# Optimization experiments

Measured on AMD Instinct MI355X. Metric: run time of the kernel, lower is better.

The kernel has to match this reference:

```python
import jax, jax.numpy as jnp
import numpy as np

D_MODEL = 1024
N_HEADS = 16
D_K = D_MODEL // N_HEADS
SEQ = 2048
BATCH = 4
THETA = 10000.0


def setup_inputs() -> dict:
    key = jax.random.key(0)
    k_x, k_q, k_k, k_v, k_o = jax.random.split(key, 5)
    std = (2.0 / (D_MODEL + D_MODEL)) ** 0.5
    def trunc(k):
        # truncated normal on [-3*std, 3*std]
        return std * jax.random.truncated_normal(k, -3.0, 3.0, (D_MODEL, D_MODEL), jnp.float32)
    return {
        "x": jax.random.normal(k_x, (BATCH, SEQ, D_MODEL), jnp.float32),
        "token_positions": jnp.arange(SEQ, dtype=jnp.int32),
        "Wq": trunc(k_q),
        "Wk": trunc(k_k),
        "Wv": trunc(k_v),
        "Wo": trunc(k_o),
    }


def _rope(x, cos, sin):
    # x: [b, h, s, d_k]; cos/sin: [s, d_k/2] broadcast over b,h
    x_even = x[..., ::2]
    x_odd = x[..., 1::2]
    out_even = x_even * cos - x_odd * sin
    out_odd = x_even * sin + x_odd * cos
    # interleave back: stack -> [..., d_k/2, 2] -> [..., d_k]
    return jnp.stack([out_even, out_odd], axis=-1).reshape(x.shape)


def reference(x, token_positions, Wq, Wk, Wv, Wo):
    B, S, D = x.shape
    H, dk = N_HEADS, D_K

    def proj(W):
        y = jnp.einsum("bsi,oi->bso", x, W)
        return y.reshape(B, S, H, dk).transpose(0, 2, 1, 3)  # b h s d

    q, k, v = proj(Wq), proj(Wk), proj(Wv)

    # RoPE caches
    freq = 1.0 / THETA ** (jnp.arange(0, dk, 2, dtype=jnp.float32) / dk)  # [dk/2]
    pos = token_positions.astype(jnp.float32)  # [S]
    freqs = pos[:, None] * freq[None, :]  # [S, dk/2]
    cos, sin = jnp.cos(freqs), jnp.sin(freqs)
    q = _rope(q, cos, sin)
    k = _rope(k, cos, sin)

    scale = 1.0 / jnp.sqrt(jnp.float32(dk))
    scores = jnp.einsum("bhqd,bhkd->bhqk", q, k) * scale  # [b,h,S,S]
    causal = jnp.tril(jnp.ones((S, S), dtype=bool))
    scores = jnp.where(causal, scores, -jnp.inf)
    # naive stable softmax (max-subtract / exp / sum), matching source
    s_max = jnp.max(scores, axis=-1, keepdims=True)
    e = jnp.exp(scores - s_max)
    attn = e / jnp.sum(e, axis=-1, keepdims=True)
    out = jnp.einsum("bhqk,bhkd->bhqd", attn, v)  # [b,h,S,dk]
    out = out.transpose(0, 2, 1, 3).reshape(B, S, D)
    return jnp.einsum("bsi,oi->bso", out, Wo)
```

## Files before the change

### kernel.cpp

```cpp
#include <hip/hip_runtime.h>

#define SEQ   2048
#define BATCH 4
#define NH    16
#define DM    1024
#define MTOT  (BATCH*SEQ)

typedef unsigned short u16;
typedef unsigned int   u32;
typedef __attribute__((ext_vector_type(8)))  __bf16 bf16x8;
typedef __attribute__((ext_vector_type(4)))  float  f32x4;
typedef __attribute__((ext_vector_type(16))) float  f32x16;
typedef __attribute__((address_space(1))) u32 as1_u32;
typedef __attribute__((address_space(3))) u32 as3_u32;

__device__ __forceinline__ u16 f2bf(float f) {
  union { float f; u32 u; } c; c.f = f;
  return (u16)((c.u + 0x7fffu + ((c.u >> 16) & 1u)) >> 16);
}

__global__ __launch_bounds__(256)
void prep_k(const float* __restrict__ x,  const float* __restrict__ Wq,
            const float* __restrict__ Wk, const float* __restrict__ Wv,
            const float* __restrict__ Wo, const int* __restrict__ pos,
            u16* __restrict__ xb,  u16* __restrict__ wqb, u16* __restrict__ wkb,
            u16* __restrict__ wvb, u16* __restrict__ wob, float2* __restrict__ tab) {
  const int NX4 = MTOT * DM / 4;
  const int NW4 = DM * DM / 4;
  const int i = blockIdx.x * blockDim.x + threadIdx.x;
  int j = i;
  const float* src = nullptr; u16* dst = nullptr;
  if (j < NX4) { src = x; dst = xb; }
  else {
    j -= NX4;
    if (j < NW4) { src = Wq; dst = wqb; }
    else if (j < 2 * NW4) { src = Wk; dst = wkb; j -= NW4; }
    else if (j < 3 * NW4) { src = Wv; dst = wvb; j -= 2 * NW4; }
    else if (j < 4 * NW4) { src = Wo; dst = wob; j -= 3 * NW4; }
    else {
      j -= 4 * NW4;
      if (j < SEQ * 32) {
        const int s = j >> 5, jj = j & 31;
        const float p = (float)pos[s];
        const float fr = powf(10000.f, -(float)jj / 32.f);
        tab[j] = make_float2(cosf(p * fr), sinf(p * fr));
      }
      return;
    }
  }
  float4 v = reinterpret_cast<const float4*>(src)[j];
  ushort4 o;
  o.x = f2bf(v.x); o.y = f2bf(v.y); o.z = f2bf(v.z); o.w = f2bf(v.w);
  reinterpret_cast<ushort4*>(dst)[j] = o;
}

template<int EPI>
__global__ __launch_bounds__(256)
void gemm_bt(const u16* __restrict__ A,
             const u16* __restrict__ B0, const u16* __restrict__ B1, const u16* __restrict__ B2,
             float* __restrict__ outF,
             u16* __restrict__ Qh, u16* __restrict__ Kh, u16* __restrict__ Vt,
             const float2* __restrict__ tab) {
  const int K = DM, N = DM;
  __shared__ u16 lsA[128 * 32];
  __shared__ u16 lsB[128 * 32];
  const int t = threadIdx.x;
  const int lane = t & 63;
  const int wid = t >> 6;
  const int wr = wid >> 1, wc = wid & 1;
  const int m0 = blockIdx.y * 128, n0 = blockIdx.x * 128;
  const int z = blockIdx.z;
  const u16* Bt = (z == 0) ? B0 : (z == 1 ? B1 : B2);

  f32x4 acc[4][4] = {};

  const int srow = t >> 2;
  const int scol = (t & 3) * 8;
  const u16* gA = A + (size_t)(m0 + srow) * K + scol;
  const u16* gB = Bt + (size_t)(n0 + srow) * K + scol;
  const u32 lo = (u32)t * 16u;

  for (int kt = 0; kt < K; kt += 32) {
    __builtin_amdgcn_global_load_lds((const as1_u32*)(gA + kt),
                                     (as3_u32*)((char*)lsA + lo), 16, 0, 0);
    __builtin_amdgcn_global_load_lds((const as1_u32*)(gA + (size_t)64 * K + kt),
                                     (as3_u32*)((char*)lsA + 4096 + lo), 16, 0, 0);
    __builtin_amdgcn_global_load_lds((const as1_u32*)(gB + kt),
                                     (as3_u32*)((char*)lsB + lo), 16, 0, 0);
    __builtin_amdgcn_global_load_lds((const as1_u32*)(gB + (size_t)64 * K + kt),
                                     (as3_u32*)((char*)lsB + 4096 + lo), 16, 0, 0);
    __syncthreads();
    bf16x8 af[4], bfr[4];
#pragma unroll
    for (int mt = 0; mt < 4; ++mt)
      af[mt] = *(const bf16x8*)&lsA[(wr * 64 + mt * 16 + (lane & 15)) * 32 + (lane >> 4) * 8];
#pragma unroll
    for (int nt = 0; nt < 4; ++nt)
      bfr[nt] = *(const bf16x8*)&lsB[(wc * 64 + nt * 16 + (lane & 15)) * 32 + (lane >> 4) * 8];
#pragma unroll
    for (int mt = 0; mt < 4; ++mt)
#pragma unroll
      for (int nt = 0; nt < 4; ++nt)
        acc[mt][nt] = __builtin_amdgcn_mfma_f32_16x16x32_bf16(af[mt], bfr[nt], acc[mt][nt], 0, 0, 0);
    __syncthreads();
  }

#pragma unroll
  for (int mt = 0; mt < 4; ++mt) {
    const int gmb = m0 + wr * 64 + mt * 16 + (lane >> 4) * 4;
#pragma unroll
    for (int nt = 0; nt < 4; ++nt) {
      const int gn = n0 + wc * 64 + nt * 16 + (lane & 15);
#pragma unroll
      for (int r = 0; r < 4; ++r) {
        float v = acc[mt][nt][r];
        if (EPI == 0) {
          outF[(size_t)(gmb + r) * N + gn] = v;
        } else {
          const int row = gmb + r;
          const int b = row >> 11, s = row & (SEQ - 1);
          const int h = gn >> 6, dd = gn & 63;
          if (z < 2) {
            float p = __shfl_xor(v, 1);
            const float2 cs = tab[(s << 5) + (dd >> 1)];
            float o = ((lane & 1) == 0) ? (v * cs.x - p * cs.y) : (p * cs.y + v * cs.x);
            if (z == 0) o *= 0.18033688011112042f;
            u16* dst = z ? Kh : Qh;
            dst[((size_t)((b * NH + h) * SEQ + s) << 6) + dd] = f2bf(o);
          } else {
            Vt[((size_t)((b * NH + h) << 6) + dd) * SEQ + s] = f2bf(v);
          }
        }
      }
    }
  }
}

__global__ __launch_bounds__(256)
void attn_k(const u16* __restrict__ Qh, const u16* __restrict__ Kh,
            const u16* __restrict__ Vt, u16* __restrict__ AO) {
  __shared__ u16 lsK[2][64 * 64];
  __shared__ u16 lsV[2][64 * 64];
  const int t = threadIdx.x, lane = t & 63, w = t >> 6;
  const int hiL = lane >> 5;
  const int q31 = lane & 31;
  const int bid = blockIdx.x;
  const int bh = bid & 63, b = bh >> 4, h = bh & 15;
  const int chunk_blk = 15 - (bid >> 6);
  const int qb_blk = chunk_blk * 128;
  const int tendB = (qb_blk + 127) >> 6;
  const int qbase = qb_blk + w * 32;
  const int tendW = (qbase + 31) >> 6;
  const u16* Qp = Qh + (size_t)bh * SEQ * 64;
  const u16* Kp = Kh + (size_t)bh * SEQ * 64;
  const u16* Vp = Vt + (size_t)bh * 64 * SEQ;

  bf16x8 qa[4];
#pragma unroll
  for (int kc = 0; kc < 4; ++kc)
    qa[kc] = *(const bf16x8*)(Qp + (size_t)(qbase + q31) * 64 + kc * 16 + hiL * 8);

  f32x16 O0 = {}, O1 = {};
  float m = -1e30f, l = 0.f;

#define STAGE(bf, kt_)                                                                  \
  {                                                                                     \
    const int k0s = (kt_) * 64;                                                         \
    _Pragma("unroll")                                                                   \
    for (int hh = 0; hh < 2; ++hh) {                                                    \
      const int idx = hh * 256 + t;                                                     \
      const int row = idx >> 3;                                                         \
      const int cb = ((idx & 7) << 4) ^ ((row & 7) << 4);                               \
      __builtin_amdgcn_global_load_lds((const as1_u32*)(Kp + (size_t)(k0s + row) * 64 + (cb >> 1)), \
                                       (as3_u32*)((char*)&lsK[bf][0] + idx * 16), 16, 0, 0); \
      __builtin_amdgcn_global_load_lds((const as1_u32*)(Vp + (size_t)row * SEQ + k0s + (cb >> 1)), \
                                       (as3_u32*)((char*)&lsV[bf][0] + idx * 16), 16, 0, 0); \
    }                                                                                   \
  }

  STAGE(0, 0)
  STAGE(1, 1)

  for (int kt = 0; kt <= tendB; ++kt) {
    const int cur = kt & 1;
    asm volatile("s_waitcnt vmcnt(4)" ::: "memory");
    __builtin_amdgcn_sched_barrier(0);
    __builtin_amdgcn_s_barrier();

    if (kt <= tendW) {
      const int k0 = kt * 64;
      const int swz = (q31 & 7) << 4;

      f32x16 S0 = {}, S1 = {};
#pragma unroll
      for (int kc = 0; kc < 4; ++kc) {
        const int cb = (kc * 32 + hiL * 16) ^ swz;
        bf16x8 ka = *(const bf16x8*)&lsK[cur][q31 * 64 + (cb >> 1)];
        S0 = __builtin_amdgcn_mfma_f32_32x32x16_bf16(ka, qa[kc], S0, 0, 0, 0);
      }
#pragma unroll
      for (int kc = 0; kc < 4; ++kc) {
        const int cb = (kc * 32 + hiL * 16) ^ swz;
        bf16x8 ka = *(const bf16x8*)&lsK[cur][(32 + q31) * 64 + (cb >> 1)];
        S1 = __builtin_amdgcn_mfma_f32_32x32x16_bf16(ka, qa[kc], S1, 0, 0, 0);
      }

      if (kt == tendW) {
        const int qg = qbase + q31;
#pragma unroll
        for (int r = 0; r < 16; ++r) {
          const int kg = k0 + (r & 3) + 8 * (r >> 2) + 4 * hiL;
          S0[r] = (kg > qg) ? -1e30f : S0[r];
          S1[r] = (kg + 32 > qg) ? -1e30f : S1[r];
        }
      }

      float vmax = -1e30f;
#pragma unroll
      for (int r = 0; r < 16; ++r) {
        vmax = fmaxf(vmax, S0[r]);
        vmax = fmaxf(vmax, S1[r]);
      }
      vmax = fmaxf(vmax, __shfl_xor(vmax, 32));

      if (vmax > m + 7.f) {
        const float al = exp2f(m - vmax);
        m = vmax; l *= al;
#pragma unroll
        for (int r = 0; r < 16; ++r) { O0[r] *= al; O1[r] *= al; }
      }

      float rs = 0.f;
#pragma unroll
      for (int r = 0; r < 16; ++r) {
        const float p0 = exp2f(S0[r] - m);
        const float p1 = exp2f(S1[r] - m);
        S0[r] = p0; S1[r] = p1;
        rs += p0 + p1;
      }
      l += rs;

      bf16x8 pb[4];
#define PACKKC(SV, kb, OUT)                                                         \
      {                                                                             \
        u32 qL0, qL1, qH0, qH1;                                                     \
        asm("v_cvt_pk_bf16_f32 %0, %1, %2" : "=v"(qL0) : "v"(SV[8*(kb)+0]), "v"(SV[8*(kb)+1])); \
        asm("v_cvt_pk_bf16_f32 %0, %1, %2" : "=v"(qL1) : "v"(SV[8*(kb)+2]), "v"(SV[8*(kb)+3])); \
        asm("v_cvt_pk_bf16_f32 %0, %1, %2" : "=v"(qH0) : "v"(SV[8*(kb)+4]), "v"(SV[8*(kb)+5])); \
        asm("v_cvt_pk_bf16_f32 %0, %1, %2" : "=v"(qH1) : "v"(SV[8*(kb)+6]), "v"(SV[8*(kb)+7])); \
        const u32 sA = hiL ? qL0 : qH0;                                             \
        const u32 sB = hiL ? qL1 : qH1;                                             \
        const u32 rA = (u32)__shfl_xor((int)sA, 32);                                \
        const u32 rB = (u32)__shfl_xor((int)sB, 32);                                \
        union { u32 wds[4]; bf16x8 v; } uu;                                         \
        uu.wds[0] = hiL ? rA : qL0;                                                 \
        uu.wds[1] = hiL ? rB : qL1;                                                 \
        uu.wds[2] = hiL ? qH0 : rA;                                                 \
        uu.wds[3] = hiL ? qH1 : rB;                                                 \
        OUT = uu.v;                                                                 \
      }
      PACKKC(S0, 0, pb[0])
      PACKKC(S0, 1, pb[1])
      PACKKC(S1, 0, pb[2])
      PACKKC(S1, 1, pb[3])
#undef PACKKC

#pragma unroll
      for (int kc = 0; kc < 4; ++kc) {
        const int cb = (kc * 32 + hiL * 16) ^ swz;
        bf16x8 va0 = *(const bf16x8*)&lsV[cur][q31 * 64 + (cb >> 1)];
        bf16x8 va1 = *(const bf16x8*)&lsV[cur][(32 + q31) * 64 + (cb >> 1)];
        O0 = __builtin_amdgcn_mfma_f32_32x32x16_bf16(va0, pb[kc], O0, 0, 0, 0);
        O1 = __builtin_amdgcn_mfma_f32_32x32x16_bf16(va1, pb[kc], O1, 0, 0, 0);
      }
    }

    __builtin_amdgcn_s_barrier();
    if (kt + 2 <= tendB) STAGE(cur, kt + 2)
  }

  l += __shfl_xor(l, 32);
  const float inv = 1.f / l;
  const int s = qbase + q31;
  u16* dst = AO + ((size_t)(b * SEQ + s) * NH + h) * 64;
#pragma unroll
  for (int rp = 0; rp < 8; ++rp) {
    const int r = rp * 2;
    const int d = (r & 3) + 8 * (r >> 2) + 4 * hiL;
    u32 w0, w1;
    asm("v_cvt_pk_bf16_f32 %0, %1, %2" : "=v"(w0) : "v"(O0[r] * inv), "v"(O0[r + 1] * inv));
    asm("v_cvt_pk_bf16_f32 %0, %1, %2" : "=v"(w1) : "v"(O1[r] * inv), "v"(O1[r + 1] * inv));
    *reinterpret_cast<u32*>(dst + d) = w0;
    *reinterpret_cast<u32*>(dst + 32 + d) = w1;
  }
}

extern "C" void kernel_launch(void* const* d_in, const int* in_sizes, int n_in,
                              void* d_out, int out_size, void* d_ws, size_t ws_size,
                              hipStream_t stream) {
  const float* x  = (const float*)d_in[0];
  const int*   pos = (const int*)d_in[1];
  const float* Wq = (const float*)d_in[2];
  const float* Wk = (const float*)d_in[3];
  const float* Wv = (const float*)d_in[4];
  const float* Wo = (const float*)d_in[5];
  float* out = (float*)d_out;
  char* ws = (char*)d_ws;
  const size_t MB = 1024 * 1024;
  if (ws_size < 73 * MB) return;

  u16* xb  = (u16*)(ws);
  u16* wqb = (u16*)(ws + 16 * MB);
  u16* wkb = (u16*)(ws + 18 * MB);
  u16* wvb = (u16*)(ws + 20 * MB);
  u16* wob = (u16*)(ws + 22 * MB);
  u16* Qh  = (u16*)(ws + 24 * MB);
  u16* Kh  = (u16*)(ws + 40 * MB);
  u16* Vt  = (u16*)(ws + 56 * MB);
  float2* tab = (float2*)(ws + 72 * MB);
  u16* AO = xb;

  const int NPREP = MTOT * DM / 4 + 4 * (DM * DM / 4) + SEQ * 32;
  prep_k<<<(NPREP + 255) / 256, 256, 0, stream>>>(x, Wq, Wk, Wv, Wo, pos,
                                                  xb, wqb, wkb, wvb, wob, tab);
  gemm_bt<1><<<dim3(8, 64, 3), 256, 0, stream>>>(xb, wqb, wkb, wvb, nullptr, Qh, Kh, Vt, tab);
  attn_k<<<dim3(1024), 256, 0, stream>>>(Qh, Kh, Vt, AO);
  gemm_bt<0><<<dim3(8, 64, 1), 256, 0, stream>>>(AO, wob, wob, wob, out, nullptr, nullptr, nullptr, nullptr);
}
```

Measured before the change: 222.4 us.

## Double-buffer GEMM LDS tiles with 64-wide K steps and XOR swizzle

```diff
diff --git a/kernel.cpp b/kernel.cpp
--- a/kernel.cpp
+++ b/kernel.cpp
@@ -62,8 +62,9 @@
              u16* __restrict__ Qh, u16* __restrict__ Kh, u16* __restrict__ Vt,
              const float2* __restrict__ tab) {
   const int K = DM, N = DM;
-  __shared__ u16 lsA[128 * 32];
-  __shared__ u16 lsB[128 * 32];
+  const int NT = K / 64;
+  __shared__ u16 lsA[2][128 * 64];
+  __shared__ u16 lsB[2][128 * 64];
   const int t = threadIdx.x;
   const int lane = t & 63;
   const int wid = t >> 6;
@@ -74,36 +75,61 @@
 
   f32x4 acc[4][4] = {};
 
-  const int srow = t >> 2;
-  const int scol = (t & 3) * 8;
-  const u16* gA = A + (size_t)(m0 + srow) * K + scol;
-  const u16* gB = Bt + (size_t)(n0 + srow) * K + scol;
-  const u32 lo = (u32)t * 16u;
-
-  for (int kt = 0; kt < K; kt += 32) {
-    __builtin_amdgcn_global_load_lds((const as1_u32*)(gA + kt),
-                                     (as3_u32*)((char*)lsA + lo), 16, 0, 0);
-    __builtin_amdgcn_global_load_lds((const as1_u32*)(gA + (size_t)64 * K + kt),
-                                     (as3_u32*)((char*)lsA + 4096 + lo), 16, 0, 0);
-    __builtin_amdgcn_global_load_lds((const as1_u32*)(gB + kt),
-                                     (as3_u32*)((char*)lsB + lo), 16, 0, 0);
-    __builtin_amdgcn_global_load_lds((const as1_u32*)(gB + (size_t)64 * K + kt),
-                                     (as3_u32*)((char*)lsB + 4096 + lo), 16, 0, 0);
-    __syncthreads();
-    bf16x8 af[4], bfr[4];
-#pragma unroll
-    for (int mt = 0; mt < 4; ++mt)
-      af[mt] = *(const bf16x8*)&lsA[(wr * 64 + mt * 16 + (lane & 15)) * 32 + (lane >> 4) * 8];
-#pragma unroll
-    for (int nt = 0; nt < 4; ++nt)
-      bfr[nt] = *(const bf16x8*)&lsB[(wc * 64 + nt * 16 + (lane & 15)) * 32 + (lane >> 4) * 8];
-#pragma unroll
-    for (int mt = 0; mt < 4; ++mt)
-#pragma unroll
-      for (int nt = 0; nt < 4; ++nt)
-        acc[mt][nt] = __builtin_amdgcn_mfma_f32_16x16x32_bf16(af[mt], bfr[nt], acc[mt][nt], 0, 0, 0);
-    __syncthreads();
-  }
+#define STG(bf, kt_)                                                                 \
+  {                                                                                  \
+    _Pragma("unroll")                                                                \
+    for (int p = 0; p < 4; ++p) {                                                    \
+      const int idx = p * 256 + t;                                                   \
+      const int row = idx >> 3;                                                      \
+      const int sg = (idx & 7) ^ (row & 7);                                          \
+      __builtin_amdgcn_global_load_lds(                                              \
+          (const as1_u32*)(A + (size_t)(m0 + row) * K + (kt_) * 64 + sg * 8),        \
+          (as3_u32*)((char*)&lsA[bf][0] + idx * 16), 16, 0, 0);                      \
+      __builtin_amdgcn_global_load_lds(                                              \
+          (const as1_u32*)(Bt + (size_t)(n0 + row) * K + (kt_) * 64 + sg * 8),       \
+          (as3_u32*)((char*)&lsB[bf][0] + idx * 16), 16, 0, 0);                      \
+    }                                                                                \
+  }
+
+  const int l15 = lane & 15, lsl = lane >> 4;
+  STG(0, 0)
+
+  for (int kt = 0; kt < NT; ++kt) {
+    const int c = kt & 1;
+    if (kt + 1 < NT) {
+      STG(c ^ 1, kt + 1)
+      asm volatile("s_waitcnt vmcnt(8)" ::: "memory");
+    } else {
+      asm volatile("s_waitcnt vmcnt(0)" ::: "memory");
+    }
+    __builtin_amdgcn_sched_barrier(0);
+    __builtin_amdgcn_s_barrier();
+
+#pragma unroll
+    for (int kk = 0; kk < 2; ++kk) {
+      bf16x8 af[4], bfr[4];
+#pragma unroll
+      for (int mt = 0; mt < 4; ++mt) {
+        const int r = wr * 64 + mt * 16 + l15;
+        af[mt] = *(const bf16x8*)((char*)&lsA[c][0] + r * 128 +
+                                  (((kk * 4 + lsl) ^ (r & 7)) << 4));
+      }
+#pragma unroll
+      for (int nt = 0; nt < 4; ++nt) {
+        const int r = wc * 64 + nt * 16 + l15;
+        bfr[nt] = *(const bf16x8*)((char*)&lsB[c][0] + r * 128 +
+                                   (((kk * 4 + lsl) ^ (r & 7)) << 4));
+      }
+#pragma unroll
+      for (int mt = 0; mt < 4; ++mt)
+#pragma unroll
+        for (int nt = 0; nt < 4; ++nt)
+          acc[mt][nt] = __builtin_amdgcn_mfma_f32_16x16x32_bf16(af[mt], bfr[nt], acc[mt][nt], 0, 0, 0);
+    }
+
+    __builtin_amdgcn_s_barrier();
+  }
+#undef STG
 
 #pragma unroll
   for (int mt = 0; mt < 4; ++mt) {
```

After: 227.3 us. 1.02x slower.
